# Kernel tuning notes

Measured on AMD Instinct MI355X. Metric: run time of the kernel, lower is better.

## Reference

```python
import jax, jax.numpy as jnp
import numpy as np

N = 50000
E = 640000
D = 128
R = 8
LAMDA = 1


def _conv(x, row, col, edge_type, coef, W, b):
    # Transform every node by every relation weight: [N, R, D]
    xW = jnp.einsum('nd,rdo->nro', x, W)
    # Gather the per-edge transformed source feature: [E, D]
    msg = xW[row, edge_type] * coef[:, None]
    # Scatter-add to target nodes, then bias
    return jax.ops.segment_sum(msg, col, num_segments=N) + b


def setup_inputs() -> dict:
    key = jax.random.key(0)
    ks = jax.random.split(key, 8)
    x = jax.random.normal(ks[0], (N, D), dtype=jnp.float32)
    edge_index = jax.random.randint(ks[1], (2, E), 0, N, dtype=jnp.int64)
    edge_type = jax.random.randint(ks[2], (E,), 0, R, dtype=jnp.int64)
    edge_weight = jax.random.uniform(ks[3], (E,), dtype=jnp.float32)
    # kaiming_uniform_(a=sqrt(5)) on [R, D, D]: bound = sqrt(6/((1+5)*fan_in)) = 1/sqrt(fan_in)
    bound = 1.0 / np.sqrt(D)
    W1 = jax.random.uniform(ks[4], (R, D, D), minval=-bound, maxval=bound, dtype=jnp.float32)
    W2 = jax.random.uniform(ks[5], (R, D, D), minval=-bound, maxval=bound, dtype=jnp.float32)
    b1 = jnp.zeros((D,), dtype=jnp.float32)
    b2 = jnp.zeros((D,), dtype=jnp.float32)
    return {"x": x, "edge_index": edge_index, "edge_type": edge_type,
            "edge_weight": edge_weight, "W1": W1, "b1": b1, "W2": W2, "b2": b2}


def reference(x, edge_index, edge_type, edge_weight, W1, b1, W2, b2):
    row = edge_index[0]  # source nodes (x_j)
    col = edge_index[1]  # target nodes (aggregation)
    deg = jax.ops.segment_sum(jnp.ones((E,), dtype=x.dtype), col, num_segments=N)
    deg_inv_sqrt = jnp.where(deg == 0, 1.0, deg ** -0.5)
    norm = deg_inv_sqrt[row] * deg_inv_sqrt[col]
    coef = norm * edge_weight  # [E]

    z1 = jax.nn.leaky_relu(_conv(x, row, col, edge_type, coef, W1, b1), negative_slope=0.01)
    # dropout is identity in eval mode
    z2 = _conv(z1, row, col, edge_type, coef, W2, b2)

    z_star = (x + z1 + z2) / 4.0
    # z_sharp = sum(temp[LAMDA:]) / (4 - LAMDA) with temp = [x, z1, z2]
    temp = [x, z1, z2]
    z_sharp = temp[LAMDA]
    for i in range(LAMDA + 1, 3):
        z_sharp = z_sharp + temp[i]
    z_sharp = z_sharp / (4.0 - LAMDA)
    return (z_star, z_sharp)
```

## Files before the change

kernel.cpp:

```cpp
#include <hip/hip_runtime.h>
#include <hip/hip_bf16.h>

#define DD 128
#define NREL 8
#define LDHB 1032
#define BC 32
#define RECCAP 1024

typedef float f32x4 __attribute__((ext_vector_type(4)));
typedef short short8 __attribute__((ext_vector_type(8)));

__device__ __forceinline__ float dis_f(float deg) {
    return deg == 0.0f ? 1.0f : rsqrtf(deg);
}

__global__ __launch_bounds__(256) void count_kernel(const int* __restrict__ ei,
                                                    int* __restrict__ cnt, int E) {
    int e = blockIdx.x * blockDim.x + threadIdx.x;
    if (e < E) atomicAdd(&cnt[ei[E + e]], 1);
}

__global__ __launch_bounds__(1024) void scan_kernel(const int* __restrict__ cnt,
                                                    int* __restrict__ cur, int N) {
    __shared__ int s[1024];
    const int t = threadIdx.x;
    const int chunk = (((N + 1023) / 1024) + 3) & ~3;
    const int beg = t * chunk, end = min(N, beg + chunk);
    int sum = 0;
    int c = beg;
    for (; c + 4 <= end; c += 4) {
        const int4 v = *(const int4*)&cnt[c];
        sum += v.x + v.y + v.z + v.w;
    }
    for (; c < end; ++c) sum += cnt[c];
    s[t] = sum;
    __syncthreads();
    for (int off = 1; off < 1024; off <<= 1) {
        int add = (t >= off) ? s[t - off] : 0;
        __syncthreads();
        s[t] += add;
        __syncthreads();
    }
    int run = s[t] - sum;
    for (int cc = beg; cc < end; ++cc) { cur[cc] = run; run += cnt[cc]; }
}

__global__ __launch_bounds__(256) void bucket_kernel(const int* __restrict__ ei,
                                                     const int* __restrict__ et,
                                                     const float* __restrict__ ew,
                                                     const int* __restrict__ cnt,
                                                     int* __restrict__ cur,
                                                     uint2* __restrict__ ebuf, int E) {
    int e = blockIdx.x * blockDim.x + threadIdx.x;
    if (e >= E) return;
    const int row = ei[e], col = ei[E + e];
    const float coef = dis_f((float)cnt[row]) * dis_f((float)cnt[col]) * ew[e];
    const int pos = atomicAdd(&cur[col], 1);
    ebuf[pos] = make_uint2(((unsigned)et[e] << 16) | (unsigned)row, __float_as_uint(coef));
}

__global__ __launch_bounds__(256) void wtrans_kernel(const float* __restrict__ W1,
                                                     const float* __restrict__ W2,
                                                     __hip_bfloat16* __restrict__ BT1,
                                                     __hip_bfloat16* __restrict__ BT2) {
    __shared__ __hip_bfloat16 tile[128][130];
    const int r = blockIdx.x & 7;
    const float* W = (blockIdx.x >> 3) ? W2 : W1;
    __hip_bfloat16* BT = (blockIdx.x >> 3) ? BT2 : BT1;
    const int o = threadIdx.x & 127;
    const int h = threadIdx.x >> 7;
    for (int d = h; d < DD; d += 2)
        tile[d][o] = __float2bfloat16(W[((size_t)r * DD + d) * DD + o]);
    __syncthreads();
    const int d = threadIdx.x & 127;
    for (int o2 = h; o2 < DD; o2 += 2)
        BT[(size_t)o2 * 1024 + r * DD + d] = tile[d][o2];
}

__global__ __launch_bounds__(256) void xcvt_kernel(const float* __restrict__ x,
                                                   __hip_bfloat16* __restrict__ xb, int total4) {
    int i = blockIdx.x * blockDim.x + threadIdx.x;
    if (i >= total4) return;
    const float4 a = ((const float4*)x)[i];
    __hip_bfloat162 p0 = __float22bfloat162_rn(make_float2(a.x, a.y));
    __hip_bfloat162 p1 = __float22bfloat162_rn(make_float2(a.z, a.w));
    uint2 u;
    u.x = *(unsigned int*)&p0;
    u.y = *(unsigned int*)&p1;
    *(uint2*)&xb[(size_t)i * 4] = u;
}

#define ACCUM(Q, MS, CF, VV) do {                                          \
    const float xl_ = __uint_as_float((VV) << 16);                         \
    const float xh_ = __uint_as_float((VV) & 0xffff0000u);                 \
    switch ((MS) >> 16) {                                                  \
        case 0: acc[Q][0]  += (CF)*xl_; acc[Q][1]  += (CF)*xh_; break;     \
        case 1: acc[Q][2]  += (CF)*xl_; acc[Q][3]  += (CF)*xh_; break;     \
        case 2: acc[Q][4]  += (CF)*xl_; acc[Q][5]  += (CF)*xh_; break;     \
        case 3: acc[Q][6]  += (CF)*xl_; acc[Q][7]  += (CF)*xh_; break;     \
        case 4: acc[Q][8]  += (CF)*xl_; acc[Q][9]  += (CF)*xh_; break;     \
        case 5: acc[Q][10] += (CF)*xl_; acc[Q][11] += (CF)*xh_; break;     \
        case 6: acc[Q][12] += (CF)*xl_; acc[Q][13] += (CF)*xh_; break;     \
        default: acc[Q][14] += (CF)*xl_; acc[Q][15] += (CF)*xh_; break;    \
    } } while (0)

template<int LAYER>
__global__ __launch_bounds__(512, 4) void fused_kernel(const __hip_bfloat16* __restrict__ srcb,
                                                       const uint2* __restrict__ ebuf,
                                                       const int* __restrict__ cur,
                                                       const __hip_bfloat16* __restrict__ BT,
                                                       const float* __restrict__ bias,
                                                       const float* __restrict__ x,
                                                       __hip_bfloat16* __restrict__ z1b,
                                                       float* __restrict__ out, int N) {
    __shared__ __hip_bfloat16 hb[BC][LDHB];
    __shared__ uint2 recs[RECCAP];
    const int tid = threadIdx.x;
    const int w = tid >> 6, l = tid & 63;
    const int c0 = blockIdx.x * BC;

    float acc[4][16];
    #pragma unroll
    for (int q = 0; q < 4; ++q)
        #pragma unroll
        for (int i = 0; i < 16; ++i) acc[q][i] = 0.f;

    const int B0 = (c0 > 0) ? cur[c0 - 1] : 0;
    const int B1 = cur[min(c0 + BC - 1, N - 1)];

    for (int cb = B0; cb < B1; cb += RECCAP) {
        const int ce = min(B1, cb + RECCAP);
        for (int i = cb + tid; i < ce; i += 512) recs[i - cb] = ebuf[i];
        __syncthreads();
        #pragma unroll
        for (int q = 0; q < 4; ++q) {
            const int c = c0 + w * 4 + q;
            if (c < N) {
                const int bc = (c > 0) ? cur[c - 1] : 0;
                const int ec = cur[c];
                const int lo = max(bc, cb), hi = min(ec, ce);
                int e = lo;
                while (e + 8 <= hi) {
                    unsigned ms[8]; float cf[8]; unsigned v[8];
                    #pragma unroll
                    for (int i = 0; i < 8; ++i) {
                        const uint2 rr = recs[e - cb + i];
                        ms[i] = (unsigned)__builtin_amdgcn_readfirstlane((int)rr.x);
                        cf[i] = __uint_as_float((unsigned)__builtin_amdgcn_readfirstlane((int)rr.y));
                    }
                    #pragma unroll
                    for (int i = 0; i < 8; ++i)
                        v[i] = *(const unsigned*)&srcb[(size_t)(ms[i] & 0xffffu) * DD + 2 * l];
                    #pragma unroll
                    for (int i = 0; i < 8; ++i) ACCUM(q, ms[i], cf[i], v[i]);
                    e += 8;
                }
                for (; e < hi; ++e) {
                    const uint2 rr = recs[e - cb];
                    const unsigned m1 = (unsigned)__builtin_amdgcn_readfirstlane((int)rr.x);
                    const float c1 = __uint_as_float((unsigned)__builtin_amdgcn_readfirstlane((int)rr.y));
                    const unsigned v1 = *(const unsigned*)&srcb[(size_t)(m1 & 0xffffu) * DD + 2 * l];
                    ACCUM(q, m1, c1, v1);
                }
            }
        }
        __syncthreads();
    }

    #pragma unroll
    for (int q = 0; q < 4; ++q) {
        const int m = w * 4 + q;
        #pragma unroll
        for (int r = 0; r < NREL; ++r) {
            __hip_bfloat162 p = __float22bfloat162_rn(make_float2(acc[q][2 * r], acc[q][2 * r + 1]));
            *(unsigned int*)&hb[m][r * DD + 2 * l] = *(unsigned int*)&p;
        }
    }
    __syncthreads();

    const int lk = (l >> 4) * 8;
    const int lr = l & 15;
    f32x4 acc0 = {0.f, 0.f, 0.f, 0.f}, acc1 = {0.f, 0.f, 0.f, 0.f};
    const __hip_bfloat16* bt = BT + (size_t)(w * 16 + lr) * 1024 + lk;
    const __hip_bfloat16* h0 = &hb[lr][lk];
    const __hip_bfloat16* h1 = &hb[16 + lr][lk];
    #pragma unroll 8
    for (int k0 = 0; k0 < 1024; k0 += 32) {
        const short8 b  = *(const short8*)(bt + k0);
        const short8 a0 = *(const short8*)(h0 + k0);
        const short8 a1 = *(const short8*)(h1 + k0);
        acc0 = __builtin_amdgcn_mfma_f32_16x16x32_bf16(a0, b, acc0, 0, 0, 0);
        acc1 = __builtin_amdgcn_mfma_f32_16x16x32_bf16(a1, b, acc1, 0, 0, 0);
    }

    const int rbase = (l >> 4) * 4;
    const int o = w * 16 + lr;
    const float bv = bias[o];
    #pragma unroll
    for (int t = 0; t < 2; ++t) {
        const f32x4 av = t ? acc1 : acc0;
        #pragma unroll
        for (int q = 0; q < 4; ++q) {
            const int c = c0 + t * 16 + rbase + q;
            if (c >= N) continue;
            const size_t idx = (size_t)c * DD + o;
            float v = av[q] + bv;
            if (LAYER == 1) {
                v = v >= 0.f ? v : 0.01f * v;
                z1b[idx] = __float2bfloat16(v);
            } else {
                const float z1v = __bfloat162float(z1b[idx]);
                const float xv2 = x[idx];
                out[idx] = (xv2 + z1v + v) * 0.25f;
                out[(size_t)N * DD + idx] = (z1v + v) * (1.f / 3.f);
            }
        }
    }
}

extern "C" void kernel_launch(void* const* d_in, const int* in_sizes, int n_in,
                              void* d_out, int out_size, void* d_ws, size_t ws_size,
                              hipStream_t stream) {
    const float* x  = (const float*)d_in[0];
    const int*   ei = (const int*)d_in[1];
    const int*   et = (const int*)d_in[2];
    const float* ew = (const float*)d_in[3];
    const float* W1 = (const float*)d_in[4];
    const float* b1 = (const float*)d_in[5];
    const float* W2 = (const float*)d_in[6];
    const float* b2 = (const float*)d_in[7];

    const int N = in_sizes[0] / DD;
    const int E = in_sizes[3];
    float* out = (float*)d_out;

    char* w = (char*)d_ws;
    int* cnt = (int*)w;                 w += (size_t)N * 4;
    int* cur = (int*)w;                 w += (size_t)N * 4;
    __hip_bfloat16* BT1 = (__hip_bfloat16*)w;  w += (size_t)DD * NREL * DD * 2;
    __hip_bfloat16* BT2 = (__hip_bfloat16*)w;  w += (size_t)DD * NREL * DD * 2;
    uint2* ebuf = (uint2*)w;            w += (size_t)E * 8;
    __hip_bfloat16* xb = (__hip_bfloat16*)w;   w += (size_t)N * DD * 2;
    __hip_bfloat16* z1b = (__hip_bfloat16*)w;

    hipMemsetAsync(cnt, 0, (size_t)N * 4, stream);

    const int eb = (E + 255) / 256;
    count_kernel<<<eb, 256, 0, stream>>>(ei, cnt, E);
    wtrans_kernel<<<16, 256, 0, stream>>>(W1, W2, BT1, BT2);
    const int t4 = N * DD / 4;
    xcvt_kernel<<<(t4 + 255) / 256, 256, 0, stream>>>(x, xb, t4);
    scan_kernel<<<1, 1024, 0, stream>>>(cnt, cur, N);
    bucket_kernel<<<eb, 256, 0, stream>>>(ei, et, ew, cnt, cur, ebuf, E);

    const int nb = (N + BC - 1) / BC;
    fused_kernel<1><<<nb, 512, 0, stream>>>(xb,  ebuf, cur, BT1, b1, x, z1b, out, N);
    fused_kernel<2><<<nb, 512, 0, stream>>>(z1b, ebuf, cur, BT2, b2, x, z1b, out, N);
}
```

Baseline: 407.8 us.

## Pad per-node edge segments to multiples of eight and use branchless relation accumulation

The CSR edge buffer now pads each target node's edge list to a multiple of eight with zero records, filled by a new fill kernel. This removes the scalar tail loop in the gather. The switch on edge type is replaced by a predicated multiply-add into all eight relation accumulators, avoiding divergent branches at the cost of eight times more FMAs per edge. The padding adds extra record loads and gathers from node 0 for zero-coefficient entries, and one more small kernel launch.

```diff
diff --git a/kernel.cpp b/kernel.cpp
--- a/kernel.cpp
+++ b/kernel.cpp
@@ -21,18 +21,14 @@
 }
 
 __global__ __launch_bounds__(1024) void scan_kernel(const int* __restrict__ cnt,
-                                                    int* __restrict__ cur, int N) {
+                                                    int* __restrict__ pstart,
+                                                    int* __restrict__ cursor, int N) {
     __shared__ int s[1024];
     const int t = threadIdx.x;
-    const int chunk = (((N + 1023) / 1024) + 3) & ~3;
+    const int chunk = (N + 1023) / 1024;
     const int beg = t * chunk, end = min(N, beg + chunk);
     int sum = 0;
-    int c = beg;
-    for (; c + 4 <= end; c += 4) {
-        const int4 v = *(const int4*)&cnt[c];
-        sum += v.x + v.y + v.z + v.w;
-    }
-    for (; c < end; ++c) sum += cnt[c];
+    for (int c = beg; c < end; ++c) sum += (cnt[c] + 7) & ~7;
     s[t] = sum;
     __syncthreads();
     for (int off = 1; off < 1024; off <<= 1) {
@@ -42,21 +38,35 @@
         __syncthreads();
     }
     int run = s[t] - sum;
-    for (int cc = beg; cc < end; ++cc) { cur[cc] = run; run += cnt[cc]; }
+    for (int c = beg; c < end; ++c) {
+        pstart[c] = run; cursor[c] = run;
+        run += (cnt[c] + 7) & ~7;
+    }
+    if (t == 1023) pstart[N] = s[1023];
 }
 
 __global__ __launch_bounds__(256) void bucket_kernel(const int* __restrict__ ei,
                                                      const int* __restrict__ et,
                                                      const float* __restrict__ ew,
                                                      const int* __restrict__ cnt,
-                                                     int* __restrict__ cur,
+                                                     int* __restrict__ cursor,
                                                      uint2* __restrict__ ebuf, int E) {
     int e = blockIdx.x * blockDim.x + threadIdx.x;
     if (e >= E) return;
     const int row = ei[e], col = ei[E + e];
     const float coef = dis_f((float)cnt[row]) * dis_f((float)cnt[col]) * ew[e];
-    const int pos = atomicAdd(&cur[col], 1);
+    const int pos = atomicAdd(&cursor[col], 1);
     ebuf[pos] = make_uint2(((unsigned)et[e] << 16) | (unsigned)row, __float_as_uint(coef));
+}
+
+__global__ __launch_bounds__(256) void fill_kernel(const int* __restrict__ cnt,
+                                                   const int* __restrict__ pstart,
+                                                   uint2* __restrict__ ebuf, int N) {
+    int idx = blockIdx.x * blockDim.x + threadIdx.x;
+    const int c = idx >> 3, j = idx & 7;
+    if (c >= N) return;
+    const int pos = pstart[c] + cnt[c] + j;
+    if (pos < pstart[c + 1]) ebuf[pos] = make_uint2(0u, 0u);
 }
 
 __global__ __launch_bounds__(256) void wtrans_kernel(const float* __restrict__ W1,
@@ -90,24 +100,10 @@
     *(uint2*)&xb[(size_t)i * 4] = u;
 }
 
-#define ACCUM(Q, MS, CF, VV) do {                                          \
-    const float xl_ = __uint_as_float((VV) << 16);                         \
-    const float xh_ = __uint_as_float((VV) & 0xffff0000u);                 \
-    switch ((MS) >> 16) {                                                  \
-        case 0: acc[Q][0]  += (CF)*xl_; acc[Q][1]  += (CF)*xh_; break;     \
-        case 1: acc[Q][2]  += (CF)*xl_; acc[Q][3]  += (CF)*xh_; break;     \
-        case 2: acc[Q][4]  += (CF)*xl_; acc[Q][5]  += (CF)*xh_; break;     \
-        case 3: acc[Q][6]  += (CF)*xl_; acc[Q][7]  += (CF)*xh_; break;     \
-        case 4: acc[Q][8]  += (CF)*xl_; acc[Q][9]  += (CF)*xh_; break;     \
-        case 5: acc[Q][10] += (CF)*xl_; acc[Q][11] += (CF)*xh_; break;     \
-        case 6: acc[Q][12] += (CF)*xl_; acc[Q][13] += (CF)*xh_; break;     \
-        default: acc[Q][14] += (CF)*xl_; acc[Q][15] += (CF)*xh_; break;    \
-    } } while (0)
-
 template<int LAYER>
 __global__ __launch_bounds__(512, 4) void fused_kernel(const __hip_bfloat16* __restrict__ srcb,
                                                        const uint2* __restrict__ ebuf,
-                                                       const int* __restrict__ cur,
+                                                       const int* __restrict__ pstart,
                                                        const __hip_bfloat16* __restrict__ BT,
                                                        const float* __restrict__ bias,
                                                        const float* __restrict__ x,
@@ -125,8 +121,8 @@
         #pragma unroll
         for (int i = 0; i < 16; ++i) acc[q][i] = 0.f;
 
-    const int B0 = (c0 > 0) ? cur[c0 - 1] : 0;
-    const int B1 = cur[min(c0 + BC - 1, N - 1)];
+    const int B0 = pstart[c0];
+    const int B1 = pstart[min(c0 + BC, N)];
 
     for (int cb = B0; cb < B1; cb += RECCAP) {
         const int ce = min(B1, cb + RECCAP);
@@ -136,31 +132,32 @@
         for (int q = 0; q < 4; ++q) {
             const int c = c0 + w * 4 + q;
             if (c < N) {
-                const int bc = (c > 0) ? cur[c - 1] : 0;
-                const int ec = cur[c];
+                const int bc = __builtin_amdgcn_readfirstlane(pstart[c]);
+                const int ec = __builtin_amdgcn_readfirstlane(pstart[c + 1]);
                 const int lo = max(bc, cb), hi = min(ec, ce);
-                int e = lo;
-                while (e + 8 <= hi) {
-                    unsigned ms[8]; float cf[8]; unsigned v[8];
+                for (int e = lo; e < hi; e += 8) {
+                    unsigned msv[8]; float cfv[8]; unsigned vv[8];
                     #pragma unroll
                     for (int i = 0; i < 8; ++i) {
                         const uint2 rr = recs[e - cb + i];
-                        ms[i] = (unsigned)__builtin_amdgcn_readfirstlane((int)rr.x);
-                        cf[i] = __uint_as_float((unsigned)__builtin_amdgcn_readfirstlane((int)rr.y));
+                        msv[i] = (unsigned)__builtin_amdgcn_readfirstlane((int)rr.x);
+                        cfv[i] = __uint_as_float((unsigned)__builtin_amdgcn_readfirstlane((int)rr.y));
                     }
                     #pragma unroll
                     for (int i = 0; i < 8; ++i)
-                        v[i] = *(const unsigned*)&srcb[(size_t)(ms[i] & 0xffffu) * DD + 2 * l];
+                        vv[i] = *(const unsigned*)&srcb[(size_t)(msv[i] & 0xffffu) * DD + 2 * l];
                     #pragma unroll
-                    for (int i = 0; i < 8; ++i) ACCUM(q, ms[i], cf[i], v[i]);
-                    e += 8;
-                }
-                for (; e < hi; ++e) {
-                    const uint2 rr = recs[e - cb];
-                    const unsigned m1 = (unsigned)__builtin_amdgcn_readfirstlane((int)rr.x);
-                    const float c1 = __uint_as_float((unsigned)__builtin_amdgcn_readfirstlane((int)rr.y));
-                    const unsigned v1 = *(const unsigned*)&srcb[(size_t)(m1 & 0xffffu) * DD + 2 * l];
-                    ACCUM(q, m1, c1, v1);
+                    for (int i = 0; i < 8; ++i) {
+                        const int etv = (int)(msv[i] >> 16);
+                        const float xl = __uint_as_float(vv[i] << 16);
+                        const float xh = __uint_as_float(vv[i] & 0xffff0000u);
+                        #pragma unroll
+                        for (int r = 0; r < NREL; ++r) {
+                            const float cr = (etv == r) ? cfv[i] : 0.f;
+                            acc[q][2 * r]     += cr * xl;
+                            acc[q][2 * r + 1] += cr * xh;
+                        }
+                    }
                 }
             }
         }
@@ -236,10 +233,11 @@
 
     char* w = (char*)d_ws;
     int* cnt = (int*)w;                 w += (size_t)N * 4;
-    int* cur = (int*)w;                 w += (size_t)N * 4;
+    int* pstart = (int*)w;              w += (size_t)(N + 16) * 4;
+    int* cursor = (int*)w;              w += (size_t)N * 4;
     __hip_bfloat16* BT1 = (__hip_bfloat16*)w;  w += (size_t)DD * NREL * DD * 2;
     __hip_bfloat16* BT2 = (__hip_bfloat16*)w;  w += (size_t)DD * NREL * DD * 2;
-    uint2* ebuf = (uint2*)w;            w += (size_t)E * 8;
+    uint2* ebuf = (uint2*)w;            w += ((size_t)E + 8 * (size_t)N) * 8;
     __hip_bfloat16* xb = (__hip_bfloat16*)w;   w += (size_t)N * DD * 2;
     __hip_bfloat16* z1b = (__hip_bfloat16*)w;
 
@@ -250,10 +248,11 @@
     wtrans_kernel<<<16, 256, 0, stream>>>(W1, W2, BT1, BT2);
     const int t4 = N * DD / 4;
     xcvt_kernel<<<(t4 + 255) / 256, 256, 0, stream>>>(x, xb, t4);
-    scan_kernel<<<1, 1024, 0, stream>>>(cnt, cur, N);
-    bucket_kernel<<<eb, 256, 0, stream>>>(ei, et, ew, cnt, cur, ebuf, E);
+    scan_kernel<<<1, 1024, 0, stream>>>(cnt, pstart, cursor, N);
+    bucket_kernel<<<eb, 256, 0, stream>>>(ei, et, ew, cnt, cursor, ebuf, E);
+    fill_kernel<<<(N * 8 + 255) / 256, 256, 0, stream>>>(cnt, pstart, ebuf, N);
 
     const int nb = (N + BC - 1) / BC;
-    fused_kernel<1><<<nb, 512, 0, stream>>>(xb,  ebuf, cur, BT1, b1, x, z1b, out, N);
-    fused_kernel<2><<<nb, 512, 0, stream>>>(z1b, ebuf, cur, BT2, b2, x, z1b, out, N);
-}
+    fused_kernel<1><<<nb, 512, 0, stream>>>(xb,  ebuf, pstart, BT1, b1, x, z1b, out, N);
+    fused_kernel<2><<<nb, 512, 0, stream>>>(z1b, ebuf, pstart, BT2, b2, x, z1b, out, N);
+}
```

After: 543.0 us. 1.33x slower.
